# Kernel tuning notes

Measured on AMD Instinct MI355X. Metric: run time of the kernel, lower is better.

The kernel has to match this reference:

```python
import jax, jax.numpy as jnp
import numpy as np
import math

D_MODEL = 1024
N_HEADS = 16
D_HEAD = D_MODEL // N_HEADS
BIAS_HIDDEN = 32
B, N = 2, 1024


def setup_inputs() -> dict:
    key = jax.random.key(0)
    ks = jax.random.split(key, 16)
    s = 1.0 / math.sqrt(D_MODEL)
    inp = {
        "x": jax.random.normal(ks[0], (B, N, D_MODEL), dtype=jnp.float32),
        "xyz": jax.random.normal(ks[1], (B, N, 3), dtype=jnp.float32),
        "Wq": jax.random.normal(ks[2], (D_MODEL, D_MODEL), jnp.float32) * s,
        "bq": jnp.zeros((D_MODEL,), jnp.float32),
        "Wk": jax.random.normal(ks[3], (D_MODEL, D_MODEL), jnp.float32) * s,
        "bk": jnp.zeros((D_MODEL,), jnp.float32),
        "Wv": jax.random.normal(ks[4], (D_MODEL, D_MODEL), jnp.float32) * s,
        "bv": jnp.zeros((D_MODEL,), jnp.float32),
        "Wo": jax.random.normal(ks[5], (D_MODEL, D_MODEL), jnp.float32) * s,
        "bo": jnp.zeros((D_MODEL,), jnp.float32),
        "W1": jax.random.normal(ks[6], (3, BIAS_HIDDEN), jnp.float32) * (1.0 / math.sqrt(3.0)),
        "b1": jnp.zeros((BIAS_HIDDEN,), jnp.float32),
        "W2": jax.random.normal(ks[7], (BIAS_HIDDEN, N_HEADS), jnp.float32) * (1.0 / math.sqrt(BIAS_HIDDEN)),
        "b2": jnp.zeros((N_HEADS,), jnp.float32),
    }
    return inp


def reference(x, xyz, Wq, bq, Wk, bk, Wv, bv, Wo, bo, W1, b1, W2, b2):
    Bv, Nv, _ = x.shape
    # q,k,v projections -> [B, H, N, Dh]
    def proj(W, b):
        return (x @ W + b).reshape(Bv, Nv, N_HEADS, D_HEAD).transpose(0, 2, 1, 3)
    q = proj(Wq, bq)
    k = proj(Wk, bk)
    v = proj(Wv, bv)
    scores = jnp.einsum('bhid,bhjd->bhij', q, k) / math.sqrt(D_HEAD)
    # pairwise relative positions -> per-head bias via tiny MLP
    rel_pos = xyz[:, :, None, :] - xyz[:, None, :, :]            # [B,N,N,3]
    hidden = jax.nn.relu(rel_pos @ W1 + b1)                      # [B,N,N,hid]
    bias = (hidden @ W2 + b2).transpose(0, 3, 1, 2)              # [B,H,N,N]
    attn = jax.nn.softmax(scores + bias, axis=-1)                # [B,H,N,N]
    out = jnp.einsum('bhij,bhjd->bhid', attn, v)                 # [B,H,N,Dh]
    out = out.transpose(0, 2, 1, 3).reshape(Bv, Nv, D_MODEL)
    out = out @ Wo + bo
    return (out, attn)
```

## Files before the change

### kernel.cpp

```cpp
#include <hip/hip_runtime.h>
#include <hip/hip_bf16.h>
#include <math.h>

#define NTOK   1024
#define DMODEL 1024
#define NHEADS 16
#define DHEAD  64

typedef __attribute__((ext_vector_type(8))) short short8;
typedef __attribute__((ext_vector_type(4))) float floatx4;
#define MFMA(a,b,c) __builtin_amdgcn_mfma_f32_16x16x32_bf16(a,b,c,0,0,0)

__device__ __forceinline__ void bf16_split(float f, ushort& h, ushort& l) {
    unsigned u = __float_as_uint(f);
    unsigned hr = (u + 0x7FFFu + ((u >> 16) & 1u)) >> 16;
    h = (ushort)hr;
    float fh = __uint_as_float(hr << 16);
    float res = f - fh;
    unsigned u2 = __float_as_uint(res);
    l = (ushort)((u2 + 0x7FFFu + ((u2 >> 16) & 1u)) >> 16);
}

__device__ __forceinline__ int swzK(int r) { return (r & 7) ^ ((r >> 3) & 7); }

__global__ __launch_bounds__(256) void bias_kernel(
    const float* __restrict__ xyz,
    const float* __restrict__ W1, const float* __restrict__ b1,
    const float* __restrict__ W2, const float* __restrict__ b2,
    float* __restrict__ attnO)
{
    __shared__ float wbuf[656];
    int tid = threadIdx.x;
    for (int i = tid; i < 656; i += 256) {
        float v;
        if (i < 96)       v = W1[i];
        else if (i < 128) v = b1[i - 96];
        else if (i < 640) v = W2[i - 128];
        else              v = b2[i - 640];
        wbuf[i] = v;
    }
    __syncthreads();
    const float* w1s = wbuf;
    const float* b1s = wbuf + 96;
    const float* w2s = wbuf + 128;
    const float* b2s = wbuf + 640;

    int j = blockIdx.x * 256 + tid;
    int i = blockIdx.y;
    int b = blockIdx.z;

    float xi0 = xyz[((size_t)b * NTOK + i) * 3 + 0];
    float xi1 = xyz[((size_t)b * NTOK + i) * 3 + 1];
    float xi2 = xyz[((size_t)b * NTOK + i) * 3 + 2];
    float d0 = xi0 - xyz[((size_t)b * NTOK + j) * 3 + 0];
    float d1 = xi1 - xyz[((size_t)b * NTOK + j) * 3 + 1];
    float d2 = xi2 - xyz[((size_t)b * NTOK + j) * 3 + 2];

    float h[32];
#pragma unroll
    for (int hh = 0; hh < 32; ++hh) {
        float v = b1s[hh] + d0 * w1s[hh] + d1 * w1s[32 + hh] + d2 * w1s[64 + hh];
        h[hh] = fmaxf(v, 0.f);
    }
    size_t base = (size_t)b * NHEADS * 1048576 + (size_t)i * 1024 + j;
#pragma unroll
    for (int hd = 0; hd < NHEADS; ++hd) {
        float acc = b2s[hd];
#pragma unroll
        for (int hh = 0; hh < 32; ++hh) acc += h[hh] * w2s[hh * 16 + hd];
        attnO[base + (size_t)hd * 1048576] = acc;
    }
}

__global__ __launch_bounds__(256) void convx_kernel(
    const float* __restrict__ x, ushort* __restrict__ xh, ushort* __restrict__ xl)
{
    int id = blockIdx.x * 256 + threadIdx.x;
    float4 v = ((const float4*)x)[id];
    ushort h0,h1,h2,h3,l0,l1,l2,l3;
    bf16_split(v.x,h0,l0); bf16_split(v.y,h1,l1);
    bf16_split(v.z,h2,l2); bf16_split(v.w,h3,l3);
    ushort4 hv; hv.x=h0; hv.y=h1; hv.z=h2; hv.w=h3;
    ushort4 lv; lv.x=l0; lv.y=l1; lv.z=l2; lv.w=l3;
    ((ushort4*)xh)[id] = hv;
    ((ushort4*)xl)[id] = lv;
}

__global__ __launch_bounds__(256) void convw_kernel(
    const float* __restrict__ Wq, const float* __restrict__ Wk,
    const float* __restrict__ Wv, const float* __restrict__ Wo,
    ushort* __restrict__ Wcth, ushort* __restrict__ Wctl,
    ushort* __restrict__ Woth, ushort* __restrict__ Wotl)
{
    __shared__ float t[64][65];
    int z = blockIdx.z;
    const float* W = (z == 0) ? Wq : (z == 1) ? Wk : (z == 2) ? Wv : Wo;
    int n0 = blockIdx.x * 64, k0 = blockIdx.y * 64;
    int tid = threadIdx.x;
    int c4 = tid & 15, rr = tid >> 4;
#pragma unroll
    for (int t4 = 0; t4 < 4; ++t4) {
        int row = rr + t4 * 16;
        float4 v = *(const float4*)&W[(size_t)(k0 + row) * 1024 + n0 + c4 * 4];
        t[row][c4 * 4 + 0] = v.x; t[row][c4 * 4 + 1] = v.y;
        t[row][c4 * 4 + 2] = v.z; t[row][c4 * 4 + 3] = v.w;
    }
    __syncthreads();
    ushort* oh = (z < 3) ? Wcth : Woth;
    ushort* ol = (z < 3) ? Wctl : Wotl;
    int nbase = (z < 3) ? z * 1024 : 0;
#pragma unroll
    for (int t4 = 0; t4 < 4; ++t4) {
        int nl = rr + t4 * 16;
        int kk = c4 * 4;
        ushort4 hv, lv;
        ushort h, l;
        bf16_split(t[kk + 0][nl], h, l); hv.x = h; lv.x = l;
        bf16_split(t[kk + 1][nl], h, l); hv.y = h; lv.y = l;
        bf16_split(t[kk + 2][nl], h, l); hv.z = h; lv.z = l;
        bf16_split(t[kk + 3][nl], h, l); hv.w = h; lv.w = l;
        size_t o = (size_t)(nbase + n0 + nl) * 1024 + k0 + kk;
        *(ushort4*)&oh[o] = hv;
        *(ushort4*)&ol[o] = lv;
    }
}

__global__ __launch_bounds__(256) void mm_kernel(
    const ushort* __restrict__ Ah, const ushort* __restrict__ Al,
    const ushort* __restrict__ Bh, const ushort* __restrict__ Bl,
    const float* __restrict__ bq, const float* __restrict__ bk,
    const float* __restrict__ bv,
    float* __restrict__ out,
    ushort* __restrict__ qh, ushort* __restrict__ ql,
    ushort* __restrict__ kh, ushort* __restrict__ kl,
    ushort* __restrict__ vth, ushort* __restrict__ vtl,
    int mode)
{
    __shared__ ushort lds[4][64][64];

    int n0 = blockIdx.x * 64;
    int m0 = blockIdx.y * 64;
    int w = threadIdx.x >> 6, l = threadIdx.x & 63;
    int li = l & 15, lg = l >> 4;
    int wm = w >> 1, wn = w & 1;

    const ushort* gbase;
    if      (w == 0) gbase = Ah + (size_t)m0 * 1024;
    else if (w == 1) gbase = Al + (size_t)m0 * 1024;
    else if (w == 2) gbase = Bh + (size_t)n0 * 1024;
    else             gbase = Bl + (size_t)n0 * 1024;
    ushort* lbase = &lds[w][0][0];
    int srow = l >> 3;
    int sc   = l & 7;

    floatx4 acc[2][2];
#pragma unroll
    for (int i = 0; i < 2; ++i)
#pragma unroll
        for (int j = 0; j < 2; ++j) acc[i][j] = (floatx4){0.f, 0.f, 0.f, 0.f};

    for (int ks = 0; ks < 16; ++ks) {
        int k0 = ks * 64;
#pragma unroll
        for (int t = 0; t < 8; ++t) {
            int rl = t * 8 + srow;
            int cs = sc ^ swzK(rl);
            const ushort* g = gbase + (size_t)rl * 1024 + k0 + cs * 8;
            __builtin_amdgcn_global_load_lds(
                (const __attribute__((address_space(1))) unsigned int*)g,
                (__attribute__((address_space(3))) unsigned int*)(lbase + t * 512),
                16, 0, 0);
        }
        __syncthreads();
#pragma unroll
        for (int kk = 0; kk < 2; ++kk) {
            short8 a[2][2], b2[2][2];
#pragma unroll
            for (int f = 0; f < 2; ++f) {
                int ra = wm * 32 + f * 16 + li;
                int ca = ((kk * 4 + lg) ^ swzK(ra)) * 8;
                a[f][0] = *(const short8*)&lds[0][ra][ca];
                a[f][1] = *(const short8*)&lds[1][ra][ca];
                int rb = wn * 32 + f * 16 + li;
                int cb = ((kk * 4 + lg) ^ swzK(rb)) * 8;
                b2[f][0] = *(const short8*)&lds[2][rb][cb];
                b2[f][1] = *(const short8*)&lds[3][rb][cb];
            }
#pragma unroll
            for (int fm = 0; fm < 2; ++fm)
#pragma unroll
                for (int fn = 0; fn < 2; ++fn) {
                    acc[fm][fn] = MFMA(a[fm][0], b2[fn][0], acc[fm][fn]);
                    acc[fm][fn] = MFMA(a[fm][0], b2[fn][1], acc[fm][fn]);
                    acc[fm][fn] = MFMA(a[fm][1], b2[fn][0], acc[fm][fn]);
                }
        }
        __syncthreads();
    }

    if (mode == 0) {
#pragma unroll
        for (int fm = 0; fm < 2; ++fm)
#pragma unroll
            for (int fn = 0; fn < 2; ++fn) {
                int col = n0 + wn * 32 + fn * 16 + li;
                float bval = bq[col];
#pragma unroll
                for (int r = 0; r < 4; ++r) {
                    int row = m0 + wm * 32 + fm * 16 + lg * 4 + r;
                    out[(size_t)row * 1024 + col] = acc[fm][fn][r] + bval;
                }
            }
    } else {
        int z = n0 >> 10;
        const float* bp = (z == 0) ? bq : (z == 1) ? bk : bv;
#pragma unroll
        for (int fm = 0; fm < 2; ++fm)
#pragma unroll
            for (int fn = 0; fn < 2; ++fn) {
                int col = n0 + wn * 32 + fn * 16 + li;
                int nloc = col & 1023;
                int hd = nloc >> 6, d = nloc & 63;
                float bval = bp[nloc];
#pragma unroll
                for (int r = 0; r < 4; ++r) {
                    int row = m0 + wm * 32 + fm * 16 + lg * 4 + r;
                    int b = row >> 10, nn = row & 1023;
                    int bh = b * NHEADS + hd;
                    float v = acc[fm][fn][r] + bval;
                    ushort h, lo; bf16_split(v, h, lo);
                    if (z == 0) {
                        size_t o = ((size_t)bh * NTOK + nn) * DHEAD + d;
                        qh[o] = h; ql[o] = lo;
                    } else if (z == 1) {
                        size_t o = ((size_t)bh * NTOK + nn) * DHEAD + d;
                        kh[o] = h; kl[o] = lo;
                    } else {
                        size_t o = ((size_t)bh * DHEAD + d) * NTOK + nn;
                        vth[o] = h; vtl[o] = lo;
                    }
                }
            }
    }
}

__global__ __launch_bounds__(256) void attn_fused_kernel(
    const ushort* __restrict__ qh, const ushort* __restrict__ ql,
    const ushort* __restrict__ kh, const ushort* __restrict__ kl,
    const ushort* __restrict__ vth, const ushort* __restrict__ vtl,
    float* __restrict__ attnO,
    ushort* __restrict__ awh, ushort* __restrict__ awl)
{
    __shared__ char smem[35328];
    float* obuf = (float*)smem;
    float* redM = (float*)(smem + 34816);
    float* redS = (float*)(smem + 35072);

    int qt = blockIdx.x, hd = blockIdx.y, b = blockIdx.z;
    int bh = b * NHEADS + hd;
    int w = threadIdx.x >> 6, l = threadIdx.x & 63;
    int li = l & 15, lg = l >> 4;

    ushort* pbh = (ushort*)smem + (size_t)w * 4352;
    ushort* pbl = pbh + 2176;

    size_t qoff = ((size_t)bh * NTOK + qt * 16 + li) * DHEAD + lg * 8;
    short8 q0h = *(const short8*)(qh + qoff);
    short8 q0l = *(const short8*)(ql + qoff);
    short8 q1h = *(const short8*)(qh + qoff + 32);
    short8 q1l = *(const short8*)(ql + qoff + 32);

    floatx4 acc[16];
#pragma unroll
    for (int jf = 0; jf < 16; ++jf) acc[jf] = (floatx4){0.f, 0.f, 0.f, 0.f};

    int jbase = w * 256;
#pragma unroll
    for (int jf = 0; jf < 16; ++jf) {
        size_t koff = ((size_t)bh * NTOK + jbase + jf * 16 + li) * DHEAD + lg * 8;
        short8 K0h = *(const short8*)(kh + koff);
        short8 K0l = *(const short8*)(kl + koff);
        short8 K1h = *(const short8*)(kh + koff + 32);
        short8 K1l = *(const short8*)(kl + koff + 32);
        acc[jf] = MFMA(q0h, K0h, acc[jf]);
        acc[jf] = MFMA(q0h, K0l, acc[jf]);
        acc[jf] = MFMA(q0l, K0h, acc[jf]);
        acc[jf] = MFMA(q1h, K1h, acc[jf]);
        acc[jf] = MFMA(q1h, K1l, acc[jf]);
        acc[jf] = MFMA(q1l, K1h, acc[jf]);
    }

    float* prow = attnO + ((size_t)bh * NTOK + qt * 16) * NTOK;

    float mloc[4] = {-1e30f, -1e30f, -1e30f, -1e30f};
#pragma unroll
    for (int jf = 0; jf < 16; ++jf)
#pragma unroll
        for (int r = 0; r < 4; ++r) {
            float s = acc[jf][r] * 0.125f
                    + prow[(size_t)(lg * 4 + r) * NTOK + jbase + jf * 16 + li];
            acc[jf][r] = s;
            mloc[r] = fmaxf(mloc[r], s);
        }
#pragma unroll
    for (int r = 0; r < 4; ++r) {
        float m = mloc[r];
        m = fmaxf(m, __shfl_xor(m, 1, 64));
        m = fmaxf(m, __shfl_xor(m, 2, 64));
        m = fmaxf(m, __shfl_xor(m, 4, 64));
        m = fmaxf(m, __shfl_xor(m, 8, 64));
        mloc[r] = m;
    }
    if (li == 0) {
#pragma unroll
        for (int r = 0; r < 4; ++r) redM[w * 16 + lg * 4 + r] = mloc[r];
    }
    __syncthreads();
    float M[4];
#pragma unroll
    for (int r = 0; r < 4; ++r) {
        int row = lg * 4 + r;
        M[r] = fmaxf(fmaxf(redM[0 + row], redM[16 + row]),
                     fmaxf(redM[32 + row], redM[48 + row]));
    }
    float sloc[4] = {0.f, 0.f, 0.f, 0.f};
#pragma unroll
    for (int jf = 0; jf < 16; ++jf)
#pragma unroll
        for (int r = 0; r < 4; ++r) {
            float e = __expf(acc[jf][r] - M[r]);
            acc[jf][r] = e;
            sloc[r] += e;
        }
#pragma unroll
    for (int r = 0; r < 4; ++r) {
        float s = sloc[r];
        s += __shfl_xor(s, 1, 64);
        s += __shfl_xor(s, 2, 64);
        s += __shfl_xor(s, 4, 64);
        s += __shfl_xor(s, 8, 64);
        sloc[r] = s;
    }
    if (li == 0) {
#pragma unroll
        for (int r = 0; r < 4; ++r) redS[w * 16 + lg * 4 + r] = sloc[r];
    }
    __syncthreads();
    float inv[4];
#pragma unroll
    for (int r = 0; r < 4; ++r) {
        int row = lg * 4 + r;
        inv[r] = 1.0f / (redS[0 + row] + redS[16 + row] +
                         redS[32 + row] + redS[48 + row]);
    }
#pragma unroll
    for (int jf = 0; jf < 16; ++jf)
#pragma unroll
        for (int r = 0; r < 4; ++r) {
            float p = acc[jf][r] * inv[r];
            acc[jf][r] = p;
            prow[(size_t)(lg * 4 + r) * NTOK + jbase + jf * 16 + li] = p;
        }

    const ushort* vbh = vth + (size_t)bh * DHEAD * NTOK;
    const ushort* vbl = vtl + (size_t)bh * DHEAD * NTOK;
    floatx4 accv[4];
#pragma unroll
    for (int nf = 0; nf < 4; ++nf) accv[nf] = (floatx4){0.f, 0.f, 0.f, 0.f};

#pragma unroll
    for (int c = 0; c < 2; ++c) {
#pragma unroll
        for (int jf8 = 0; jf8 < 8; ++jf8) {
            int jf = c * 8 + jf8;
            int kloc = jf8 * 16 + li;
#pragma unroll
            for (int r = 0; r < 4; ++r) {
                int row = lg * 4 + r;
                ushort hh, ll; bf16_split(acc[jf][r], hh, ll);
                pbh[row * 136 + kloc] = hh;
                pbl[row * 136 + kloc] = ll;
            }
        }
#pragma unroll
        for (int ks = 0; ks < 4; ++ks) {
            int koff_l = ks * 32 + lg * 8;
            short8 Ah8 = *(const short8*)&pbh[li * 136 + koff_l];
            short8 Al8 = *(const short8*)&pbl[li * 136 + koff_l];
            size_t kg = (size_t)jbase + c * 128 + koff_l;
#pragma unroll
            for (int nf = 0; nf < 4; ++nf) {
                short8 Bh8 = *(const short8*)(vbh + (size_t)(nf * 16 + li) * NTOK + kg);
                short8 Bl8 = *(const short8*)(vbl + (size_t)(nf * 16 + li) * NTOK + kg);
                accv[nf] = MFMA(Ah8, Bh8, accv[nf]);
                accv[nf] = MFMA(Ah8, Bl8, accv[nf]);
                accv[nf] = MFMA(Al8, Bh8, accv[nf]);
            }
        }
    }

    __syncthreads();
#pragma unroll
    for (int nf = 0; nf < 4; ++nf)
#pragma unroll
        for (int r = 0; r < 4; ++r)
            obuf[(w * 16 + lg * 4 + r) * 68 + nf * 16 + li] = accv[nf][r];
    __syncthreads();
    {
        int row = threadIdx.x >> 4, d0 = (threadIdx.x & 15) * 4;
        float s0 = 0.f, s1 = 0.f, s2 = 0.f, s3 = 0.f;
#pragma unroll
        for (int ww = 0; ww < 4; ++ww) {
            float4 t = *(const float4*)&obuf[(ww * 16 + row) * 68 + d0];
            s0 += t.x; s1 += t.y; s2 += t.z; s3 += t.w;
        }
        ushort4 hv, lv; ushort h, lo;
        bf16_split(s0, h, lo); hv.x = h; lv.x = lo;
        bf16_split(s1, h, lo); hv.y = h; lv.y = lo;
        bf16_split(s2, h, lo); hv.z = h; lv.z = lo;
        bf16_split(s3, h, lo); hv.w = h; lv.w = lo;
        size_t o = ((size_t)(b * NTOK + qt * 16 + row)) * DMODEL + hd * DHEAD + d0;
        *(ushort4*)&awh[o] = hv;
        *(ushort4*)&awl[o] = lv;
    }
}

extern "C" void kernel_launch(void* const* d_in, const int* in_sizes, int n_in,
                              void* d_out, int out_size, void* d_ws, size_t ws_size,
                              hipStream_t stream)
{
    const float* x   = (const float*)d_in[0];
    const float* xyz = (const float*)d_in[1];
    const float* Wq  = (const float*)d_in[2];
    const float* bq  = (const float*)d_in[3];
    const float* Wk  = (const float*)d_in[4];
    const float* bk  = (const float*)d_in[5];
    const float* Wv  = (const float*)d_in[6];
    const float* bv  = (const float*)d_in[7];
    const float* Wo  = (const float*)d_in[8];
    const float* bo  = (const float*)d_in[9];
    const float* W1  = (const float*)d_in[10];
    const float* b1  = (const float*)d_in[11];
    const float* W2  = (const float*)d_in[12];
    const float* b2  = (const float*)d_in[13];

    const size_t OUT_ELEMS = (size_t)2 * NTOK * DMODEL;
    float* out   = (float*)d_out;
    float* attnO = out + OUT_ELEMS;

    char* ws = (char*)d_ws;
    ushort* Wcth = (ushort*)(ws);
    ushort* Wctl = (ushort*)(ws + 6291456);
    ushort* Woth = (ushort*)(ws + 12582912);
    ushort* Wotl = (ushort*)(ws + 14680064);
    ushort* qh   = (ushort*)(ws + 16777216);
    ushort* ql   = (ushort*)(ws + 20971520);
    ushort* kh   = (ushort*)(ws + 25165824);
    ushort* kl   = (ushort*)(ws + 29360128);
    ushort* vth  = (ushort*)(ws + 33554432);
    ushort* vtl  = (ushort*)(ws + 37748736);
    ushort* xh   = (ushort*)(ws + 41943040);
    ushort* xl   = (ushort*)(ws + 46137344);
    ushort* awh  = xh;
    ushort* awl  = xl;

    bias_kernel<<<dim3(4, 1024, 2), 256, 0, stream>>>(xyz, W1, b1, W2, b2, attnO);
    convx_kernel<<<dim3(2048), 256, 0, stream>>>(x, xh, xl);
    convw_kernel<<<dim3(16, 16, 4), 256, 0, stream>>>(Wq, Wk, Wv, Wo,
                                                      Wcth, Wctl, Woth, Wotl);
    mm_kernel<<<dim3(48, 32), 256, 0, stream>>>(xh, xl, Wcth, Wctl,
                                                bq, bk, bv, nullptr,
                                                qh, ql, kh, kl, vth, vtl, 1);
    attn_fused_kernel<<<dim3(64, NHEADS, 2), 256, 0, stream>>>(
        qh, ql, kh, kl, vth, vtl, attnO, awh, awl);
    mm_kernel<<<dim3(16, 32), 256, 0, stream>>>(awh, awl, Woth, Wotl,
                                                bo, bo, bo, out,
                                                nullptr, nullptr, nullptr, nullptr,
                                                nullptr, nullptr, 0);
}
```

Before: 441.1 us.

## Compute transposed S tile so P feeds PV MFMA directly from registers

Swaps the MFMA operands for QK^T and permutes the K rows each lane loads, so every lane ends up holding scores for one query row across 8 contiguous key columns. The result register layout matches the A-operand layout of the PV MFMA, so the LDS staging of P (bf16 hi/lo writes, then reads) is removed. Bias reads and probability writes become float4-vectorised along the row. Row reductions now need only two cross-lane shuffles, at the cost of a more intricate index mapping.

```diff
diff --git a/kernel.cpp b/kernel.cpp
--- a/kernel.cpp
+++ b/kernel.cpp
@@ -251,18 +251,15 @@
     float* __restrict__ attnO,
     ushort* __restrict__ awh, ushort* __restrict__ awl)
 {
-    __shared__ char smem[35328];
-    float* obuf = (float*)smem;
-    float* redM = (float*)(smem + 34816);
-    float* redS = (float*)(smem + 35072);
+    __shared__ float obuf[4 * 16 * 68];
+    __shared__ float redM[4][16];
+    __shared__ float redS[4][16];
 
     int qt = blockIdx.x, hd = blockIdx.y, b = blockIdx.z;
     int bh = b * NHEADS + hd;
     int w = threadIdx.x >> 6, l = threadIdx.x & 63;
     int li = l & 15, lg = l >> 4;
-
-    ushort* pbh = (ushort*)smem + (size_t)w * 4352;
-    ushort* pbl = pbh + 2176;
+    int jbase = w * 256;
 
     size_t qoff = ((size_t)bh * NTOK + qt * 16 + li) * DHEAD + lg * 8;
     short8 q0h = *(const short8*)(qh + qoff);
@@ -274,93 +271,65 @@
 #pragma unroll
     for (int jf = 0; jf < 16; ++jf) acc[jf] = (floatx4){0.f, 0.f, 0.f, 0.f};
 
-    int jbase = w * 256;
-#pragma unroll
-    for (int jf = 0; jf < 16; ++jf) {
-        size_t koff = ((size_t)bh * NTOK + jbase + jf * 16 + li) * DHEAD + lg * 8;
-        short8 K0h = *(const short8*)(kh + koff);
-        short8 K0l = *(const short8*)(kl + koff);
-        short8 K1h = *(const short8*)(kh + koff + 32);
-        short8 K1l = *(const short8*)(kl + koff + 32);
-        acc[jf] = MFMA(q0h, K0h, acc[jf]);
-        acc[jf] = MFMA(q0h, K0l, acc[jf]);
-        acc[jf] = MFMA(q0l, K0h, acc[jf]);
-        acc[jf] = MFMA(q1h, K1h, acc[jf]);
-        acc[jf] = MFMA(q1h, K1l, acc[jf]);
-        acc[jf] = MFMA(q1l, K1h, acc[jf]);
-    }
+#pragma unroll
+    for (int t = 0; t < 8; ++t)
+#pragma unroll
+        for (int half = 0; half < 2; ++half) {
+            int jf = t * 2 + half;
+            int krow = jbase + t * 32 + ((li >> 2) << 3) + half * 4 + (li & 3);
+            size_t koff = ((size_t)bh * NTOK + krow) * DHEAD + lg * 8;
+            short8 K0h = *(const short8*)(kh + koff);
+            short8 K0l = *(const short8*)(kl + koff);
+            short8 K1h = *(const short8*)(kh + koff + 32);
+            short8 K1l = *(const short8*)(kl + koff + 32);
+            acc[jf] = MFMA(K0h, q0h, acc[jf]);
+            acc[jf] = MFMA(K0h, q0l, acc[jf]);
+            acc[jf] = MFMA(K0l, q0h, acc[jf]);
+            acc[jf] = MFMA(K1h, q1h, acc[jf]);
+            acc[jf] = MFMA(K1h, q1l, acc[jf]);
+            acc[jf] = MFMA(K1l, q1h, acc[jf]);
+        }
 
     float* prow = attnO + ((size_t)bh * NTOK + qt * 16) * NTOK;
 
-    float mloc[4] = {-1e30f, -1e30f, -1e30f, -1e30f};
+    float m = -1e30f;
+#pragma unroll
+    for (int t = 0; t < 8; ++t) {
+        const float* bp = prow + (size_t)li * NTOK + jbase + t * 32 + lg * 8;
+        float4 ba = *(const float4*)bp;
+        float4 bb = *(const float4*)(bp + 4);
+        float bav[4] = {ba.x, ba.y, ba.z, ba.w};
+        float bbv[4] = {bb.x, bb.y, bb.z, bb.w};
+#pragma unroll
+        for (int r = 0; r < 4; ++r) {
+            float s0 = acc[2 * t][r] * 0.125f + bav[r];
+            float s1 = acc[2 * t + 1][r] * 0.125f + bbv[r];
+            acc[2 * t][r] = s0;
+            acc[2 * t + 1][r] = s1;
+            m = fmaxf(m, fmaxf(s0, s1));
+        }
+    }
+    m = fmaxf(m, __shfl_xor(m, 16, 64));
+    m = fmaxf(m, __shfl_xor(m, 32, 64));
+    if (lg == 0) redM[w][li] = m;
+    __syncthreads();
+    float M = fmaxf(fmaxf(redM[0][li], redM[1][li]),
+                    fmaxf(redM[2][li], redM[3][li]));
+
+    float s = 0.f;
 #pragma unroll
     for (int jf = 0; jf < 16; ++jf)
 #pragma unroll
         for (int r = 0; r < 4; ++r) {
-            float s = acc[jf][r] * 0.125f
-                    + prow[(size_t)(lg * 4 + r) * NTOK + jbase + jf * 16 + li];
-            acc[jf][r] = s;
-            mloc[r] = fmaxf(mloc[r], s);
-        }
-#pragma unroll
-    for (int r = 0; r < 4; ++r) {
-        float m = mloc[r];
-        m = fmaxf(m, __shfl_xor(m, 1, 64));
-        m = fmaxf(m, __shfl_xor(m, 2, 64));
-        m = fmaxf(m, __shfl_xor(m, 4, 64));
-        m = fmaxf(m, __shfl_xor(m, 8, 64));
-        mloc[r] = m;
-    }
-    if (li == 0) {
-#pragma unroll
-        for (int r = 0; r < 4; ++r) redM[w * 16 + lg * 4 + r] = mloc[r];
-    }
+            float e = __expf(acc[jf][r] - M);
+            acc[jf][r] = e;
+            s += e;
+        }
+    s += __shfl_xor(s, 16, 64);
+    s += __shfl_xor(s, 32, 64);
+    if (lg == 0) redS[w][li] = s;
     __syncthreads();
-    float M[4];
-#pragma unroll
-    for (int r = 0; r < 4; ++r) {
-        int row = lg * 4 + r;
-        M[r] = fmaxf(fmaxf(redM[0 + row], redM[16 + row]),
-                     fmaxf(redM[32 + row], redM[48 + row]));
-    }
-    float sloc[4] = {0.f, 0.f, 0.f, 0.f};
-#pragma unroll
-    for (int jf = 0; jf < 16; ++jf)
-#pragma unroll
-        for (int r = 0; r < 4; ++r) {
-            float e = __expf(acc[jf][r] - M[r]);
-            acc[jf][r] = e;
-            sloc[r] += e;
-        }
-#pragma unroll
-    for (int r = 0; r < 4; ++r) {
-        float s = sloc[r];
-        s += __shfl_xor(s, 1, 64);
-        s += __shfl_xor(s, 2, 64);
-        s += __shfl_xor(s, 4, 64);
-        s += __shfl_xor(s, 8, 64);
-        sloc[r] = s;
-    }
-    if (li == 0) {
-#pragma unroll
-        for (int r = 0; r < 4; ++r) redS[w * 16 + lg * 4 + r] = sloc[r];
-    }
-    __syncthreads();
-    float inv[4];
-#pragma unroll
-    for (int r = 0; r < 4; ++r) {
-        int row = lg * 4 + r;
-        inv[r] = 1.0f / (redS[0 + row] + redS[16 + row] +
-                         redS[32 + row] + redS[48 + row]);
-    }
-#pragma unroll
-    for (int jf = 0; jf < 16; ++jf)
-#pragma unroll
-        for (int r = 0; r < 4; ++r) {
-            float p = acc[jf][r] * inv[r];
-            acc[jf][r] = p;
-            prow[(size_t)(lg * 4 + r) * NTOK + jbase + jf * 16 + li] = p;
-        }
+    float inv = 1.0f / (redS[0][li] + redS[1][li] + redS[2][li] + redS[3][li]);
 
     const ushort* vbh = vth + (size_t)bh * DHEAD * NTOK;
     const ushort* vbl = vtl + (size_t)bh * DHEAD * NTOK;
@@ -369,37 +338,37 @@
     for (int nf = 0; nf < 4; ++nf) accv[nf] = (floatx4){0.f, 0.f, 0.f, 0.f};
 
 #pragma unroll
-    for (int c = 0; c < 2; ++c) {
-#pragma unroll
-        for (int jf8 = 0; jf8 < 8; ++jf8) {
-            int jf = c * 8 + jf8;
-            int kloc = jf8 * 16 + li;
-#pragma unroll
-            for (int r = 0; r < 4; ++r) {
-                int row = lg * 4 + r;
-                ushort hh, ll; bf16_split(acc[jf][r], hh, ll);
-                pbh[row * 136 + kloc] = hh;
-                pbl[row * 136 + kloc] = ll;
-            }
-        }
-#pragma unroll
-        for (int ks = 0; ks < 4; ++ks) {
-            int koff_l = ks * 32 + lg * 8;
-            short8 Ah8 = *(const short8*)&pbh[li * 136 + koff_l];
-            short8 Al8 = *(const short8*)&pbl[li * 136 + koff_l];
-            size_t kg = (size_t)jbase + c * 128 + koff_l;
-#pragma unroll
-            for (int nf = 0; nf < 4; ++nf) {
-                short8 Bh8 = *(const short8*)(vbh + (size_t)(nf * 16 + li) * NTOK + kg);
-                short8 Bl8 = *(const short8*)(vbl + (size_t)(nf * 16 + li) * NTOK + kg);
-                accv[nf] = MFMA(Ah8, Bh8, accv[nf]);
-                accv[nf] = MFMA(Ah8, Bl8, accv[nf]);
-                accv[nf] = MFMA(Al8, Bh8, accv[nf]);
-            }
-        }
-    }
-
-    __syncthreads();
+    for (int t = 0; t < 8; ++t) {
+        float pa[4], pb[4];
+#pragma unroll
+        for (int r = 0; r < 4; ++r) {
+            pa[r] = acc[2 * t][r] * inv;
+            pb[r] = acc[2 * t + 1][r] * inv;
+        }
+        float* pw = prow + (size_t)li * NTOK + jbase + t * 32 + lg * 8;
+        *(float4*)pw = make_float4(pa[0], pa[1], pa[2], pa[3]);
+        *(float4*)(pw + 4) = make_float4(pb[0], pb[1], pb[2], pb[3]);
+
+        short8 Ah8, Al8;
+#pragma unroll
+        for (int e = 0; e < 4; ++e) {
+            ushort hh, ll;
+            bf16_split(pa[e], hh, ll); Ah8[e] = (short)hh; Al8[e] = (short)ll;
+            bf16_split(pb[e], hh, ll); Ah8[4 + e] = (short)hh; Al8[4 + e] = (short)ll;
+        }
+        size_t kg = (size_t)jbase + t * 32 + lg * 8;
+#pragma unroll
+        for (int nf = 0; nf < 4; ++nf) {
+            const ushort* vph = vbh + (size_t)(nf * 16 + li) * NTOK + kg;
+            const ushort* vpl = vbl + (size_t)(nf * 16 + li) * NTOK + kg;
+            short8 Bh8 = *(const short8*)vph;
+            short8 Bl8 = *(const short8*)vpl;
+            accv[nf] = MFMA(Ah8, Bh8, accv[nf]);
+            accv[nf] = MFMA(Ah8, Bl8, accv[nf]);
+            accv[nf] = MFMA(Al8, Bh8, accv[nf]);
+        }
+    }
+
 #pragma unroll
     for (int nf = 0; nf < 4; ++nf)
 #pragma unroll
```

Measured after the change: 438.3 us. About the same (-0.6%).
